# Optimization experiments

Hardware: AMD Instinct MI355X
Metric: run time of the kernel (lower is better)

## Reference

```python
import jax, jax.numpy as jnp
import numpy as np

N_HEADS = 16
WINDOW = 256  # window_size; keep keys with |i-j| <= WINDOW//2


def setup_inputs() -> dict:
    key = jax.random.key(0)
    ks = jax.random.split(key, 6)
    B, S, D = 2, 2048, 1024
    x = jax.random.normal(ks[0], (B, S, D), dtype=jnp.float32)
    # torch nn.Linear weights are [out_features, in_features]
    scale = 1.0 / np.sqrt(D)
    Wq = jax.random.normal(ks[1], (D, D), dtype=jnp.float32) * scale
    Wk = jax.random.normal(ks[2], (D, D), dtype=jnp.float32) * scale
    Wv = jax.random.normal(ks[3], (D, D), dtype=jnp.float32) * scale
    Wo = jax.random.normal(ks[4], (D, D), dtype=jnp.float32) * scale
    # standard ALiBi slopes: 2^(-8*(h+1)/H)
    slopes = jnp.asarray(2.0 ** (-8.0 * (np.arange(1, N_HEADS + 1) / N_HEADS)), dtype=jnp.float32)
    return {"x": x, "Wq": Wq, "Wk": Wk, "Wv": Wv, "Wo": Wo, "slopes": slopes}


def reference(x, Wq, Wk, Wv, Wo, slopes):
    B, S, D = x.shape
    H = N_HEADS
    dk = D // H
    # projections (torch Linear: y = x @ W.T)
    q = jnp.einsum('bsd,od->bso', x, Wq).reshape(B, S, H, dk)
    k = jnp.einsum('bsd,od->bso', x, Wk).reshape(B, S, H, dk)
    v = jnp.einsum('bsd,od->bso', x, Wv).reshape(B, S, H, dk)
    # full score matrix [B,H,S,S]
    scores = jnp.einsum('bqhd,bkhd->bhqk', q, k) / jnp.sqrt(jnp.asarray(dk, x.dtype))
    pos = jnp.arange(S)
    rel = (pos[:, None] - pos[None, :]).astype(x.dtype)          # [S,S] q_pos - k_pos
    scores = scores + slopes[None, :, None, None] * rel[None, None]
    window_mask = jnp.abs(pos[:, None] - pos[None, :]) <= (WINDOW // 2)  # [S,S]
    scores = jnp.where(window_mask[None, None], scores, -jnp.inf)
    attn = jax.nn.softmax(scores, axis=-1)
    out = jnp.einsum('bhqk,bkhd->bqhd', attn, v).reshape(B, S, D)
    return jnp.einsum('bsd,od->bso', out, Wo)
```

## Files before the change

### kernel.cpp

```cpp
#include <hip/hip_runtime.h>
#include <hip/hip_bf16.h>

#define S_LEN   2048
#define D_MODEL 1024
#define NH      16
#define DK      64
#define BATCH   2
#define M_ROWS  (BATCH * S_LEN)
#define LDP     72
#define LDV     66
#define LDW     132

typedef __attribute__((ext_vector_type(8))) short bf16x8;
typedef __attribute__((ext_vector_type(4))) float f32x4;
typedef __attribute__((ext_vector_type(8))) unsigned short us8;
typedef __attribute__((ext_vector_type(4))) unsigned short us4;

static __device__ __forceinline__ float b2f(unsigned short s) {
    unsigned u = ((unsigned)s) << 16;
    return __builtin_bit_cast(float, u);
}
static __device__ __forceinline__ unsigned short f2bf(float f) {
    unsigned u = __builtin_bit_cast(unsigned, f);
    u += 0x7fffu + ((u >> 16) & 1u);
    return (unsigned short)(u >> 16);
}

__global__ __launch_bounds__(256) void cvt_all(const float* __restrict__ x,
                                               const float* __restrict__ wq,
                                               const float* __restrict__ wk,
                                               const float* __restrict__ wv,
                                               const float* __restrict__ wo,
                                               unsigned short* __restrict__ dst) {
    const int b = blockIdx.x;
    if (b < 2048) {
        const size_t o8 = (size_t)b * 256 + threadIdx.x;
        const float4* s = (const float4*)x + o8 * 2;
        float4 a = s[0], bb = s[1];
        us8 o;
        o[0] = f2bf(a.x);  o[1] = f2bf(a.y);  o[2] = f2bf(a.z);  o[3] = f2bf(a.w);
        o[4] = f2bf(bb.x); o[5] = f2bf(bb.y); o[6] = f2bf(bb.z); o[7] = f2bf(bb.w);
        *((us8*)dst + o8) = o;
    } else {
        const int wi = (b - 2048) >> 9;
        const float* src = (wi == 0) ? wq : (wi == 1) ? wk : (wi == 2) ? wv : wo;
        const size_t local = (size_t)((b - 2048) & 511) * 256 + threadIdx.x;
        const float4* s = (const float4*)src + local * 2;
        float4 a = s[0], bb = s[1];
        us8 o;
        o[0] = f2bf(a.x);  o[1] = f2bf(a.y);  o[2] = f2bf(a.z);  o[3] = f2bf(a.w);
        o[4] = f2bf(bb.x); o[5] = f2bf(bb.y); o[6] = f2bf(bb.z); o[7] = f2bf(bb.w);
        *((us8*)dst + 524288 + (size_t)wi * 131072 + local) = o;
    }
}

template <int STORE_BF16, int BN>
__global__ __launch_bounds__(256) void mfma_gemm_bt(const unsigned short* __restrict__ A,
                                                    const unsigned short* __restrict__ W,
                                                    void* __restrict__ Cv, int N) {
    constexpr int K = 1024, BM = 128, BK = 64;
    constexpr int MI = (BN == 128) ? 4 : 2;
    constexpr int SMEM = (STORE_BF16 && BN == 128) ? (128 * LDW)
                                                   : (BM * BK + BN * BK);
    __shared__ unsigned short smem[SMEM];
    unsigned short* As = smem;
    unsigned short* Bs = smem + BM * BK;

    const int tid  = threadIdx.x;
    const int w    = tid >> 6;
    const int lane = tid & 63;
    const int m0 = blockIdx.y * BM;
    const int n0 = blockIdx.x * BN;
    const int wr = (BN == 128) ? (w >> 1) * 64 : w * 32;
    const int wc = (BN == 128) ? (w & 1) * 64 : 0;

    const int srow   = lane >> 3;
    const int schunk = ((lane & 7) ^ (lane >> 3)) * 8;
    const int sw = lane & 7;
    const int c0 = (((lane >> 4) + 0) ^ sw) * 8;
    const int c1 = (((lane >> 4) + 4) ^ sw) * 8;

    f32x4 acc[MI][4] = {};

    for (int k0 = 0; k0 < K; k0 += BK) {
        __syncthreads();
#pragma unroll
        for (int t = 0; t < 4; ++t) {
            const int rbase = w * 32 + t * 8;
            const unsigned short* ga = A + (size_t)(m0 + rbase + srow) * K + k0 + schunk;
            __builtin_amdgcn_global_load_lds(
                (const __attribute__((address_space(1))) void*)ga,
                (__attribute__((address_space(3))) void*)(As + rbase * BK), 16, 0, 0);
        }
#pragma unroll
        for (int t = 0; t < BN / 32; ++t) {
            const int rbase = w * (BN / 4) + t * 8;
            const unsigned short* gb = W + (size_t)(n0 + rbase + srow) * K + k0 + schunk;
            __builtin_amdgcn_global_load_lds(
                (const __attribute__((address_space(1))) void*)gb,
                (__attribute__((address_space(3))) void*)(Bs + rbase * BK), 16, 0, 0);
        }
        __syncthreads();

        const int fr = lane & 15;
#pragma unroll
        for (int kk = 0; kk < 2; ++kk) {
            const int co = kk ? c1 : c0;
            bf16x8 af[MI], bfr[4];
#pragma unroll
            for (int i = 0; i < MI; ++i)
                af[i] = *(const bf16x8*)(As + (wr + i * 16 + fr) * BK + co);
#pragma unroll
            for (int j = 0; j < 4; ++j)
                bfr[j] = *(const bf16x8*)(Bs + (wc + j * 16 + fr) * BK + co);
#pragma unroll
            for (int i = 0; i < MI; ++i)
#pragma unroll
                for (int j = 0; j < 4; ++j)
                    acc[i][j] = __builtin_amdgcn_mfma_f32_16x16x32_bf16(af[i], bfr[j], acc[i][j], 0, 0, 0);
        }
    }

    const int col = lane & 15;
    const int rq  = (lane >> 4) * 4;

    if constexpr (STORE_BF16 && BN == 128) {
        __syncthreads();
#pragma unroll
        for (int i = 0; i < 4; ++i)
#pragma unroll
            for (int j = 0; j < 4; ++j)
#pragma unroll
                for (int r = 0; r < 4; ++r)
                    smem[(wr + i * 16 + rq + r) * LDW + wc + j * 16 + col] = f2bf(acc[i][j][r]);
        __syncthreads();
#pragma unroll
        for (int e = 0; e < 8; ++e) {
            const int idx = e * 256 + tid;
            const int row = idx >> 4;
            const int cc  = (idx & 15) * 8;
            us4 lo = *(const us4*)(smem + row * LDW + cc);
            us4 hi = *(const us4*)(smem + row * LDW + cc + 4);
            us8 v;
            v[0] = lo[0]; v[1] = lo[1]; v[2] = lo[2]; v[3] = lo[3];
            v[4] = hi[0]; v[5] = hi[1]; v[6] = hi[2]; v[7] = hi[3];
            *(us8*)((unsigned short*)Cv + (size_t)(m0 + row) * N + n0 + cc) = v;
        }
    } else {
#pragma unroll
        for (int i = 0; i < MI; ++i)
#pragma unroll
            for (int j = 0; j < 4; ++j)
#pragma unroll
                for (int r = 0; r < 4; ++r) {
                    const int gm = m0 + wr + i * 16 + rq + r;
                    const int gn = n0 + wc + j * 16 + col;
                    if (STORE_BF16)
                        ((unsigned short*)Cv)[(size_t)gm * N + gn] = f2bf(acc[i][j][r]);
                    else
                        ((float*)Cv)[(size_t)gm * N + gn] = acc[i][j][r];
                }
    }
}

__global__ __launch_bounds__(256) void attn_mfma(const unsigned short* __restrict__ qkvb,
                                                 const float* __restrict__ slopes,
                                                 unsigned short* __restrict__ aoutb) {
    __shared__ unsigned short QPs[64 * LDP];
    __shared__ unsigned short Ks[64 * 64];
    __shared__ unsigned short Vt[64 * LDV];

    const int tid  = threadIdx.x;
    const int w    = tid >> 6;
    const int lane = tid & 63;
    const int q0 = blockIdx.x * 64;
    const int h  = blockIdx.y;
    const int b  = blockIdx.z;
    const float slope = slopes[h];
    const size_t rowbase = (size_t)b * S_LEN * 3072;

#pragma unroll
    for (int e = 0; e < 2; ++e) {
        int idx = e * 256 + tid;
        int r = idx >> 3, cc = (idx & 7) * 8;
        us8 v = *(const us8*)(qkvb + rowbase + (size_t)(q0 + r) * 3072 + h * DK + cc);
        *(us8*)(QPs + r * LDP + cc) = v;
    }

    const int col = lane & 15;
    const int rq  = (lane >> 4) * 4;
    const int wq  = w * 16;
    const int fo  = (lane >> 4) * 8;

    const int srowK   = lane >> 3;
    const int schunkK = ((lane & 7) ^ srowK) * 8;
    const int kc0 = (((lane >> 4) + 0) ^ (lane & 7)) * 8;
    const int kc1 = (((lane >> 4) + 4) ^ (lane & 7)) * 8;

    __syncthreads();
    const bf16x8 aq0 = *(const bf16x8*)(QPs + (wq + col) * LDP + fo);
    const bf16x8 aq1 = *(const bf16x8*)(QPs + (wq + col) * LDP + fo + 32);

    float mrow[4];
#pragma unroll
    for (int r = 0; r < 4; ++r) {
        const int qpos = q0 + wq + rq + r;
        mrow[r] = slope * (float)(qpos < 128 ? qpos : 128) + 12.0f;
    }

    f32x4 o_acc[4] = {};
    float l_part[4] = {0.f, 0.f, 0.f, 0.f};

    const unsigned short* kbase = qkvb + rowbase + 1024 + h * DK;
    const unsigned short* vbase0 = qkvb + rowbase + 2048 + h * DK;

    for (int c = 0; c < 5; ++c) {
        const int k0 = q0 - 128 + c * 64;
        __syncthreads();

#pragma unroll
        for (int t = 0; t < 2; ++t) {
            const int rbase = w * 16 + t * 8;
            const unsigned short* gk = kbase + (long long)(k0 + rbase + srowK) * 3072 + schunkK;
            __builtin_amdgcn_global_load_lds(
                (const __attribute__((address_space(1))) void*)gk,
                (__attribute__((address_space(3))) void*)(Ks + rbase * 64), 16, 0, 0);
        }
        {
            const int rp = tid >> 3;
            const int cc = (tid & 7) * 8;
            const unsigned short* vb = vbase0 + cc;
            const long long kp0 = (long long)(k0 + rp * 2);
            us8 v0 = *(const us8*)(vb + kp0 * 3072);
            us8 v1 = *(const us8*)(vb + (kp0 + 1) * 3072);
#pragma unroll
            for (int t = 0; t < 8; ++t) {
                unsigned pk = (unsigned)(unsigned short)v0[t] | ((unsigned)(unsigned short)v1[t] << 16);
                *(unsigned*)(Vt + (cc + t) * LDV + rp * 2) = pk;
            }
        }
        __syncthreads();

        f32x4 sacc[4] = {};
#pragma unroll
        for (int j = 0; j < 4; ++j) {
            bf16x8 bk0 = *(const bf16x8*)(Ks + (j * 16 + col) * 64 + kc0);
            bf16x8 bk1 = *(const bf16x8*)(Ks + (j * 16 + col) * 64 + kc1);
            sacc[j] = __builtin_amdgcn_mfma_f32_16x16x32_bf16(aq0, bk0, sacc[j], 0, 0, 0);
            sacc[j] = __builtin_amdgcn_mfma_f32_16x16x32_bf16(aq1, bk1, sacc[j], 0, 0, 0);
        }

#pragma unroll
        for (int j = 0; j < 4; ++j) {
            const int kpos = k0 + j * 16 + col;
            const bool kin = (unsigned)kpos < (unsigned)S_LEN;
#pragma unroll
            for (int r = 0; r < 4; ++r) {
                const int rel = (q0 + wq + rq + r) - kpos;
                const bool ok = kin && (rel <= 128) && (rel >= -128);
                float p = 0.f;
                if (ok)
                    p = __expf(fmaf(sacc[j][r], 0.125f, slope * (float)rel - mrow[r]));
                l_part[r] += p;
                QPs[(wq + rq + r) * LDP + j * 16 + col] = f2bf(p);
            }
        }

        {
            bf16x8 ap0 = *(const bf16x8*)(QPs + (wq + col) * LDP + fo);
            bf16x8 ap1 = *(const bf16x8*)(QPs + (wq + col) * LDP + fo + 32);
#pragma unroll
            for (int j = 0; j < 4; ++j) {
                bf16x8 bv0 = *(const bf16x8*)(Vt + (j * 16 + col) * LDV + fo);
                bf16x8 bv1 = *(const bf16x8*)(Vt + (j * 16 + col) * LDV + fo + 32);
                o_acc[j] = __builtin_amdgcn_mfma_f32_16x16x32_bf16(ap0, bv0, o_acc[j], 0, 0, 0);
                o_acc[j] = __builtin_amdgcn_mfma_f32_16x16x32_bf16(ap1, bv1, o_acc[j], 0, 0, 0);
            }
        }
    }

    float inv[4];
#pragma unroll
    for (int r = 0; r < 4; ++r) {
        float l = l_part[r];
#pragma unroll
        for (int off = 1; off < 16; off <<= 1) l += __shfl_xor(l, off, 64);
        inv[r] = 1.f / l;
    }

#pragma unroll
    for (int j = 0; j < 4; ++j)
#pragma unroll
        for (int r = 0; r < 4; ++r) {
            const int qpos = q0 + wq + rq + r;
            aoutb[((size_t)b * S_LEN + qpos) * D_MODEL + h * DK + j * 16 + col] =
                f2bf(o_acc[j][r] * inv[r]);
        }
}

extern "C" void kernel_launch(void* const* d_in, const int* in_sizes, int n_in,
                              void* d_out, int out_size, void* d_ws, size_t ws_size,
                              hipStream_t stream) {
    const float* x      = (const float*)d_in[0];
    const float* Wq     = (const float*)d_in[1];
    const float* Wk     = (const float*)d_in[2];
    const float* Wv     = (const float*)d_in[3];
    const float* Wo     = (const float*)d_in[4];
    const float* slopes = (const float*)d_in[5];
    float* out = (float*)d_out;

    unsigned short* xb    = (unsigned short*)d_ws;
    unsigned short* wb    = xb    + (size_t)M_ROWS * D_MODEL;
    unsigned short* wob   = wb    + (size_t)3072 * D_MODEL;
    unsigned short* qkvb  = wob   + (size_t)1024 * D_MODEL;
    unsigned short* aoutb = qkvb  + (size_t)M_ROWS * 3072;

    dim3 blk(256);
    cvt_all<<<4096, blk, 0, stream>>>(x, Wq, Wk, Wv, Wo, xb);
    mfma_gemm_bt<1, 128><<<dim3(3072 / 128, M_ROWS / 128), blk, 0, stream>>>(xb, wb, qkvb, 3072);
    attn_mfma<<<dim3(S_LEN / 64, NH, BATCH), blk, 0, stream>>>(qkvb, slopes, aoutb);
    mfma_gemm_bt<0, 64><<<dim3(1024 / 64, M_ROWS / 128), blk, 0, stream>>>(aoutb, wob, out, 1024);
}
```

Baseline: 158.6 us.

## Enlarge attention query tile to 128 rows with 128-key chunks

The attention kernel now handles 128 queries per block instead of 64. Each warp covers 32 query rows, and keys/values are streamed in three 128-wide chunks instead of five 64-wide ones. This cuts the redundant band of keys computed per query, from 320 to 384 keys shared across twice as many queries, and improves K/V reuse from shared memory. The grid order is also changed so heads and batch vary fastest, which may help L2 locality. In exchange each block uses more registers and LDS and has fewer blocks to schedule.

```diff
diff --git a/kernel.cpp b/kernel.cpp
--- a/kernel.cpp
+++ b/kernel.cpp
@@ -7,8 +7,10 @@
 #define DK      64
 #define BATCH   2
 #define M_ROWS  (BATCH * S_LEN)
+#define QT      128
 #define LDP     72
-#define LDV     66
+#define LDP2    136
+#define LDV2    130
 #define LDW     132
 
 typedef __attribute__((ext_vector_type(8))) short bf16x8;
@@ -16,10 +18,6 @@
 typedef __attribute__((ext_vector_type(8))) unsigned short us8;
 typedef __attribute__((ext_vector_type(4))) unsigned short us4;
 
-static __device__ __forceinline__ float b2f(unsigned short s) {
-    unsigned u = ((unsigned)s) << 16;
-    return __builtin_bit_cast(float, u);
-}
 static __device__ __forceinline__ unsigned short f2bf(float f) {
     unsigned u = __builtin_bit_cast(unsigned, f);
     u += 0x7fffu + ((u >> 16) & 1u);
@@ -166,21 +164,21 @@
 __global__ __launch_bounds__(256) void attn_mfma(const unsigned short* __restrict__ qkvb,
                                                  const float* __restrict__ slopes,
                                                  unsigned short* __restrict__ aoutb) {
-    __shared__ unsigned short QPs[64 * LDP];
-    __shared__ unsigned short Ks[64 * 64];
-    __shared__ unsigned short Vt[64 * LDV];
+    __shared__ unsigned short QPs[QT * LDP2];
+    __shared__ unsigned short Ks[QT * 64];
+    __shared__ unsigned short Vt[64 * LDV2];
 
     const int tid  = threadIdx.x;
     const int w    = tid >> 6;
     const int lane = tid & 63;
-    const int q0 = blockIdx.x * 64;
-    const int h  = blockIdx.y;
-    const int b  = blockIdx.z;
+    const int h  = blockIdx.x;
+    const int b  = blockIdx.y;
+    const int q0 = blockIdx.z * QT;
     const float slope = slopes[h];
     const size_t rowbase = (size_t)b * S_LEN * 3072;
 
 #pragma unroll
-    for (int e = 0; e < 2; ++e) {
+    for (int e = 0; e < 4; ++e) {
         int idx = e * 256 + tid;
         int r = idx >> 3, cc = (idx & 7) * 8;
         us8 v = *(const us8*)(qkvb + rowbase + (size_t)(q0 + r) * 3072 + h * DK + cc);
@@ -189,7 +187,7 @@
 
     const int col = lane & 15;
     const int rq  = (lane >> 4) * 4;
-    const int wq  = w * 16;
+    const int wq  = w * 32;
     const int fo  = (lane >> 4) * 8;
 
     const int srowK   = lane >> 3;
@@ -198,104 +196,124 @@
     const int kc1 = (((lane >> 4) + 4) ^ (lane & 7)) * 8;
 
     __syncthreads();
-    const bf16x8 aq0 = *(const bf16x8*)(QPs + (wq + col) * LDP + fo);
-    const bf16x8 aq1 = *(const bf16x8*)(QPs + (wq + col) * LDP + fo + 32);
-
-    float mrow[4];
-#pragma unroll
-    for (int r = 0; r < 4; ++r) {
-        const int qpos = q0 + wq + rq + r;
-        mrow[r] = slope * (float)(qpos < 128 ? qpos : 128) + 12.0f;
-    }
-
-    f32x4 o_acc[4] = {};
-    float l_part[4] = {0.f, 0.f, 0.f, 0.f};
-
-    const unsigned short* kbase = qkvb + rowbase + 1024 + h * DK;
+    bf16x8 aq[2][2];
+#pragma unroll
+    for (int m = 0; m < 2; ++m) {
+        aq[m][0] = *(const bf16x8*)(QPs + (wq + m * 16 + col) * LDP + fo);
+        aq[m][1] = *(const bf16x8*)(QPs + (wq + m * 16 + col) * LDP + fo + 32);
+    }
+
+    float mrow[2][4];
+#pragma unroll
+    for (int m = 0; m < 2; ++m)
+#pragma unroll
+        for (int r = 0; r < 4; ++r) {
+            const int qpos = q0 + wq + m * 16 + rq + r;
+            mrow[m][r] = slope * (float)(qpos < 128 ? qpos : 128) + 12.0f;
+        }
+
+    f32x4 o_acc[2][4] = {};
+    float l_part[2][4] = {};
+
+    const unsigned short* kbase  = qkvb + rowbase + 1024 + h * DK;
     const unsigned short* vbase0 = qkvb + rowbase + 2048 + h * DK;
 
-    for (int c = 0; c < 5; ++c) {
-        const int k0 = q0 - 128 + c * 64;
-        __syncthreads();
-
-#pragma unroll
-        for (int t = 0; t < 2; ++t) {
-            const int rbase = w * 16 + t * 8;
+    for (int c = 0; c < 3; ++c) {
+        const int k0 = q0 - 128 + c * 128;
+        __syncthreads();
+
+#pragma unroll
+        for (int t = 0; t < 4; ++t) {
+            const int rbase = w * 32 + t * 8;
             const unsigned short* gk = kbase + (long long)(k0 + rbase + srowK) * 3072 + schunkK;
             __builtin_amdgcn_global_load_lds(
                 (const __attribute__((address_space(1))) void*)gk,
                 (__attribute__((address_space(3))) void*)(Ks + rbase * 64), 16, 0, 0);
         }
-        {
+#pragma unroll
+        for (int e = 0; e < 2; ++e) {
             const int rp = tid >> 3;
             const int cc = (tid & 7) * 8;
+            const long long kk = (long long)(k0 + 64 * e + 2 * rp);
             const unsigned short* vb = vbase0 + cc;
-            const long long kp0 = (long long)(k0 + rp * 2);
-            us8 v0 = *(const us8*)(vb + kp0 * 3072);
-            us8 v1 = *(const us8*)(vb + (kp0 + 1) * 3072);
+            us8 v0 = *(const us8*)(vb + kk * 3072);
+            us8 v1 = *(const us8*)(vb + (kk + 1) * 3072);
 #pragma unroll
             for (int t = 0; t < 8; ++t) {
                 unsigned pk = (unsigned)(unsigned short)v0[t] | ((unsigned)(unsigned short)v1[t] << 16);
-                *(unsigned*)(Vt + (cc + t) * LDV + rp * 2) = pk;
+                *(unsigned*)(Vt + (cc + t) * LDV2 + 64 * e + 2 * rp) = pk;
             }
         }
         __syncthreads();
 
-        f32x4 sacc[4] = {};
-#pragma unroll
-        for (int j = 0; j < 4; ++j) {
+        f32x4 sacc[2][8] = {};
+#pragma unroll
+        for (int j = 0; j < 8; ++j) {
             bf16x8 bk0 = *(const bf16x8*)(Ks + (j * 16 + col) * 64 + kc0);
             bf16x8 bk1 = *(const bf16x8*)(Ks + (j * 16 + col) * 64 + kc1);
-            sacc[j] = __builtin_amdgcn_mfma_f32_16x16x32_bf16(aq0, bk0, sacc[j], 0, 0, 0);
-            sacc[j] = __builtin_amdgcn_mfma_f32_16x16x32_bf16(aq1, bk1, sacc[j], 0, 0, 0);
-        }
-
-#pragma unroll
-        for (int j = 0; j < 4; ++j) {
-            const int kpos = k0 + j * 16 + col;
-            const bool kin = (unsigned)kpos < (unsigned)S_LEN;
+#pragma unroll
+            for (int m = 0; m < 2; ++m) {
+                sacc[m][j] = __builtin_amdgcn_mfma_f32_16x16x32_bf16(aq[m][0], bk0, sacc[m][j], 0, 0, 0);
+                sacc[m][j] = __builtin_amdgcn_mfma_f32_16x16x32_bf16(aq[m][1], bk1, sacc[m][j], 0, 0, 0);
+            }
+        }
+
+#pragma unroll
+        for (int m = 0; m < 2; ++m)
+#pragma unroll
+            for (int j = 0; j < 8; ++j) {
+                const int kpos = k0 + j * 16 + col;
+                const bool kin = (unsigned)kpos < (unsigned)S_LEN;
+#pragma unroll
+                for (int r = 0; r < 4; ++r) {
+                    const int rel = (q0 + wq + m * 16 + rq + r) - kpos;
+                    const bool ok = kin && (rel <= 128) && (rel >= -128);
+                    float p = 0.f;
+                    if (ok)
+                        p = __expf(fmaf(sacc[m][j][r], 0.125f, slope * (float)rel - mrow[m][r]));
+                    l_part[m][r] += p;
+                    QPs[(wq + m * 16 + rq + r) * LDP2 + j * 16 + col] = f2bf(p);
+                }
+            }
+
+        {
+            bf16x8 ap[2][4];
+#pragma unroll
+            for (int m = 0; m < 2; ++m)
+#pragma unroll
+                for (int t = 0; t < 4; ++t)
+                    ap[m][t] = *(const bf16x8*)(QPs + (wq + m * 16 + col) * LDP2 + 32 * t + fo);
+#pragma unroll
+            for (int j4 = 0; j4 < 4; ++j4)
+#pragma unroll
+                for (int t = 0; t < 4; ++t) {
+                    bf16x8 bv = *(const bf16x8*)(Vt + (j4 * 16 + col) * LDV2 + 32 * t + fo);
+#pragma unroll
+                    for (int m = 0; m < 2; ++m)
+                        o_acc[m][j4] = __builtin_amdgcn_mfma_f32_16x16x32_bf16(ap[m][t], bv, o_acc[m][j4], 0, 0, 0);
+                }
+        }
+    }
+
+#pragma unroll
+    for (int m = 0; m < 2; ++m) {
+        float inv[4];
+#pragma unroll
+        for (int r = 0; r < 4; ++r) {
+            float l = l_part[m][r];
+#pragma unroll
+            for (int off = 1; off < 16; off <<= 1) l += __shfl_xor(l, off, 64);
+            inv[r] = 1.f / l;
+        }
+#pragma unroll
+        for (int j4 = 0; j4 < 4; ++j4)
 #pragma unroll
             for (int r = 0; r < 4; ++r) {
-                const int rel = (q0 + wq + rq + r) - kpos;
-                const bool ok = kin && (rel <= 128) && (rel >= -128);
-                float p = 0.f;
-                if (ok)
-                    p = __expf(fmaf(sacc[j][r], 0.125f, slope * (float)rel - mrow[r]));
-                l_part[r] += p;
-                QPs[(wq + rq + r) * LDP + j * 16 + col] = f2bf(p);
+                const int qpos = q0 + wq + m * 16 + rq + r;
+                aoutb[((size_t)b * S_LEN + qpos) * D_MODEL + h * DK + j4 * 16 + col] =
+                    f2bf(o_acc[m][j4][r] * inv[r]);
             }
-        }
-
-        {
-            bf16x8 ap0 = *(const bf16x8*)(QPs + (wq + col) * LDP + fo);
-            bf16x8 ap1 = *(const bf16x8*)(QPs + (wq + col) * LDP + fo + 32);
-#pragma unroll
-            for (int j = 0; j < 4; ++j) {
-                bf16x8 bv0 = *(const bf16x8*)(Vt + (j * 16 + col) * LDV + fo);
-                bf16x8 bv1 = *(const bf16x8*)(Vt + (j * 16 + col) * LDV + fo + 32);
-                o_acc[j] = __builtin_amdgcn_mfma_f32_16x16x32_bf16(ap0, bv0, o_acc[j], 0, 0, 0);
-                o_acc[j] = __builtin_amdgcn_mfma_f32_16x16x32_bf16(ap1, bv1, o_acc[j], 0, 0, 0);
-            }
-        }
-    }
-
-    float inv[4];
-#pragma unroll
-    for (int r = 0; r < 4; ++r) {
-        float l = l_part[r];
-#pragma unroll
-        for (int off = 1; off < 16; off <<= 1) l += __shfl_xor(l, off, 64);
-        inv[r] = 1.f / l;
-    }
-
-#pragma unroll
-    for (int j = 0; j < 4; ++j)
-#pragma unroll
-        for (int r = 0; r < 4; ++r) {
-            const int qpos = q0 + wq + rq + r;
-            aoutb[((size_t)b * S_LEN + qpos) * D_MODEL + h * DK + j * 16 + col] =
-                f2bf(o_acc[j][r] * inv[r]);
-        }
+    }
 }
 
 extern "C" void kernel_launch(void* const* d_in, const int* in_sizes, int n_in,
@@ -318,6 +336,6 @@
     dim3 blk(256);
     cvt_all<<<4096, blk, 0, stream>>>(x, Wq, Wk, Wv, Wo, xb);
     mfma_gemm_bt<1, 128><<<dim3(3072 / 128, M_ROWS / 128), blk, 0, stream>>>(xb, wb, qkvb, 3072);
-    attn_mfma<<<dim3(S_LEN / 64, NH, BATCH), blk, 0, stream>>>(qkvb, slopes, aoutb);
+    attn_mfma<<<dim3(NH, BATCH, S_LEN / QT), blk, 0, stream>>>(qkvb, slopes, aoutb);
     mfma_gemm_bt<0, 64><<<dim3(1024 / 64, M_ROWS / 128), blk, 0, stream>>>(aoutb, wob, out, 1024);
 }
```

Result: no change. 160.3 us (+1.0%).
